# Performance work log

Measured on AMD Instinct MI355X. Metric: run time of the kernel, lower is better.

## Reference

```python
import jax, jax.numpy as jnp
import numpy as np

B, N, K, OUT = 8, 2048, 30, 13


def _knn_idx(x, k):
    # x: [B,N,F] -> indices of k nearest neighbors (squared L2, includes self)
    sq = jnp.sum(x * x, axis=-1)  # [B,N]
    d = sq[:, :, None] + sq[:, None, :] - 2.0 * jnp.einsum('bnf,bmf->bnm', x, x)
    _, idx = jax.lax.top_k(-d, k)  # [B,N,k]
    return idx


def _edge_conv(x, W1, b1, g, be, W2, b2, k):
    # DynamicEdgeConv: kNN on feature space, message = MLP([x_i, x_j - x_i]), max aggr
    idx = _knn_idx(x, k)                                  # [B,N,k] (non-differentiable)
    xj = jax.vmap(lambda xb, ib: xb[ib])(x, idx)          # gather neighbors [B,N,k,F]
    xi = x[:, :, None, :]
    e = jnp.concatenate([jnp.broadcast_to(xi, xj.shape), xj - xi], axis=-1)  # [B,N,k,2F]
    # PyG MLP([2F,64,64]): Linear + BN(eval: affine) + ReLU, then plain Linear
    h = jax.nn.relu((e @ W1 + b1) * g + be)
    h = h @ W2 + b2
    return jnp.max(h, axis=2)                             # max over k neighbors -> [B,N,64]


def setup_inputs():
    key = jax.random.key(0)
    ks = jax.random.split(key, 40)

    def lin(i, fin, fout):
        W = jax.random.normal(ks[i], (fin, fout), jnp.float32) / np.sqrt(fin)
        return W, jnp.zeros((fout,), jnp.float32)

    inp = {}
    inp['x'] = jax.random.normal(ks[0], (B, N, 3), jnp.float32)
    inp['pos'] = jax.random.normal(ks[1], (B, N, 3), jnp.float32)
    inp['batch'] = jnp.repeat(jnp.arange(B, dtype=jnp.int32), N)
    i = 2
    for name, fin in [('c1', 12), ('c2', 128), ('c3', 128)]:
        W1, b1 = lin(i, fin, 64); i += 1
        W2, b2 = lin(i, 64, 64); i += 1
        inp[name + '_W1'] = W1; inp[name + '_b1'] = b1
        inp[name + '_g'] = 1.0 + 0.1 * jax.random.normal(ks[i], (64,), jnp.float32); i += 1
        inp[name + '_be'] = 0.1 * jax.random.normal(ks[i], (64,), jnp.float32); i += 1
        inp[name + '_W2'] = W2; inp[name + '_b2'] = b2
    dims = [192, 1024, 256, 128, OUT]
    for j in range(4):
        W, b = lin(i, dims[j], dims[j + 1]); i += 1
        inp[f'm_W{j + 1}'] = W; inp[f'm_b{j + 1}'] = b
    return inp


def reference(x, pos, batch,
              c1_W1, c1_b1, c1_g, c1_be, c1_W2, c1_b2,
              c2_W1, c2_b1, c2_g, c2_be, c2_W2, c2_b2,
              c3_W1, c3_b1, c3_g, c3_be, c3_W2, c3_b2,
              m_W1, m_b1, m_W2, m_b2, m_W3, m_b3, m_W4, m_b4):
    x0 = jnp.concatenate([pos, x], axis=-1)               # [B,N,6]
    x1 = _edge_conv(x0, c1_W1, c1_b1, c1_g, c1_be, c1_W2, c1_b2, K)
    x2 = _edge_conv(x1, c2_W1, c2_b1, c2_g, c2_be, c2_W2, c2_b2, K)
    x3 = _edge_conv(x2, c3_W1, c3_b1, c3_g, c3_be, c3_W2, c3_b2, K)
    h = jnp.concatenate([x1, x2, x3], axis=-1)            # [B,N,192]
    # classifier MLP([192,1024,256,128,OUT], norm=None): Linear+ReLU(+dropout=eval id), plain last
    h = jax.nn.relu(h @ m_W1 + m_b1)
    h = jax.nn.relu(h @ m_W2 + m_b2)
    h = jax.nn.relu(h @ m_W3 + m_b3)
    out = h @ m_W4 + m_b4
    return jax.nn.log_softmax(out, axis=-1), x3
```

## Files before the change

kernel.cpp:

```cpp
#include <hip/hip_runtime.h>

using u16 = unsigned short;
using u32 = unsigned int;
typedef short s8v __attribute__((ext_vector_type(8)));
typedef short s4v __attribute__((ext_vector_type(4)));
typedef float f4v __attribute__((ext_vector_type(4)));

#define DEV static __device__ __forceinline__

DEV void cvt_split(float f, u16& h, u16& l) {
  u32 x = __builtin_bit_cast(u32, f);
  u32 rh = (x + 0x7FFFu + ((x >> 16) & 1u)) & 0xFFFF0000u;
  h = (u16)(rh >> 16);
  float fl = f - __builtin_bit_cast(float, rh);
  u32 y = __builtin_bit_cast(u32, fl);
  l = (u16)((y + 0x7FFFu + ((y >> 16) & 1u)) >> 16);
}

__global__ void k_misc0(const float* __restrict__ x, const float* __restrict__ pos,
                        float* __restrict__ x0,
                        const float* __restrict__ W2c3, u16* __restrict__ eW2h, u16* __restrict__ eW2l,
                        const float* __restrict__ W2c1, const float* __restrict__ W2c2,
                        float* __restrict__ W2T1, float* __restrict__ W2T2) {
  int b = blockIdx.x;
  if (b < 64) {
    int p = b * 256 + threadIdx.x;
    float* o = x0 + (size_t)p * 8;
    o[0] = pos[p*3+0]; o[1] = pos[p*3+1]; o[2] = pos[p*3+2];
    o[3] = x[p*3+0];   o[4] = x[p*3+1];   o[5] = x[p*3+2];
    o[6] = 0.f; o[7] = 0.f;
  } else if (b < 80) {
    int e = (b - 64) * 256 + threadIdx.x;
    int k = e >> 6, n = e & 63;
    u16 h, l;
    cvt_split(W2c3[e], h, l);
    eW2h[n*72 + k] = h;
    eW2l[n*72 + k] = l;
  } else {
    const float* src = (b == 80) ? W2c1 : W2c2;
    float* dst = (b == 80) ? W2T1 : W2T2;
    for (int e = threadIdx.x; e < 4096; e += 256) {
      int c = e >> 6, cp = e & 63;
      dst[cp*64 + c] = src[e];
    }
  }
}

__global__ void k_splitmlp(const float* __restrict__ W1, const float* __restrict__ W2,
                           const float* __restrict__ W3,
                           u16* __restrict__ m1h, u16* __restrict__ m1l,
                           u16* __restrict__ m2h, u16* __restrict__ m2l,
                           u16* __restrict__ m3h, u16* __restrict__ m3l) {
  int b = blockIdx.x;
  u16 h, l;
  if (b < 768) {
    int e = b * 256 + threadIdx.x;
    if (e < 192 * 1024) {
      int k = e >> 10, n = e & 1023;
      cvt_split(W1[e], h, l);
      m1h[(size_t)n*200 + k] = h; m1l[(size_t)n*200 + k] = l;
    }
  } else if (b < 1792) {
    int e = (b - 768) * 256 + threadIdx.x;
    int k = e >> 8, n = e & 255;
    cvt_split(W2[e], h, l);
    m2h[(size_t)n*1032 + k] = h; m2l[(size_t)n*1032 + k] = l;
  } else {
    int e = (b - 1792) * 256 + threadIdx.x;
    int k = e >> 7, n = e & 127;
    cvt_split(W3[e], h, l);
    m3h[(size_t)n*264 + k] = h; m3l[(size_t)n*264 + k] = l;
  }
}

__global__ void k_sqnorm(const float* __restrict__ x, int stride, int F,
                         float* __restrict__ sq) {
  int wid  = (blockIdx.x * 256 + threadIdx.x) >> 6;
  int lane = threadIdx.x & 63;
  float v = (lane < F) ? x[(size_t)wid * stride + lane] : 0.f;
  float s = v * v;
  #pragma unroll
  for (int m = 32; m; m >>= 1) s += __shfl_xor(s, m);
  if (lane == 0) sq[wid] = s;
}

template<int F>
__global__ __launch_bounds__(256) void k_dist(const float* __restrict__ x, int stride,
    const float* __restrict__ sq, int cbase, float* __restrict__ D) {
  constexpr int PAD = F + 4;
  __shared__ __align__(16) float Xi[128 * PAD];
  __shared__ __align__(16) float Xj[128 * PAD];
  __shared__ float SQI[128], SQJ[128];
  int b  = blockIdx.z;
  int i0 = cbase + blockIdx.y * 128;
  int j0 = blockIdx.x * 128;
  int tid = threadIdx.x;
  constexpr int NPASS = 128 * (F / 4) / 256;
  #pragma unroll
  for (int ps = 0; ps < NPASS; ++ps) {
    int e4 = ps * 256 + tid;
    int r = e4 / (F / 4), f4 = (e4 % (F / 4)) * 4;
    *(float4*)&Xi[r*PAD + f4] = *(const float4*)&x[(size_t)(b*2048 + i0 + r)*stride + f4];
    *(float4*)&Xj[r*PAD + f4] = *(const float4*)&x[(size_t)(b*2048 + j0 + r)*stride + f4];
  }
  if (tid < 128) {
    SQI[tid] = sq[b*2048 + i0 + tid];
    SQJ[tid] = sq[b*2048 + j0 + tid];
  }
  __syncthreads();
  int tx = tid & 15, ty = tid >> 4;
  float acc[8][8];
  #pragma unroll
  for (int i = 0; i < 8; ++i)
    #pragma unroll
    for (int j = 0; j < 8; ++j) acc[i][j] = 0.f;
  #pragma unroll 2
  for (int kf = 0; kf < F; kf += 4) {
    float4 av[8], wv[8];
    #pragma unroll
    for (int i = 0; i < 8; ++i) av[i] = *(const float4*)&Xi[(ty + 16*i)*PAD + kf];
    #pragma unroll
    for (int j = 0; j < 8; ++j) wv[j] = *(const float4*)&Xj[(tx + 16*j)*PAD + kf];
    #pragma unroll
    for (int i = 0; i < 8; ++i)
      #pragma unroll
      for (int j = 0; j < 8; ++j) {
        acc[i][j] += av[i].x * wv[j].x;
        acc[i][j] += av[i].y * wv[j].y;
        acc[i][j] += av[i].z * wv[j].z;
        acc[i][j] += av[i].w * wv[j].w;
      }
  }
  #pragma unroll
  for (int i = 0; i < 8; ++i) {
    int row = ty + 16*i;
    float si = SQI[row];
    #pragma unroll
    for (int j = 0; j < 8; ++j) {
      int col = tx + 16*j;
      D[(size_t)(b*512 + blockIdx.y*128 + row)*2048 + j0 + col] =
          si + SQJ[col] - 2.f * acc[i][j];
    }
  }
}

__global__ __launch_bounds__(256) void k_topk(const float* __restrict__ D, int cbase,
                                              int* __restrict__ knn) {
  int wid  = blockIdx.x * 4 + (threadIdx.x >> 6);
  int lane = threadIdx.x & 63;
  int b = wid >> 9, il = wid & 511;
  const float* row = D + (size_t)(b*512 + il) * 2048;
  float v[32];
  #pragma unroll
  for (int s = 0; s < 32; ++s) v[s] = row[lane + 64*s];
  const float INFV = __builtin_bit_cast(float, 0x7f800000u);
  int wj = 0;
  #pragma unroll 1
  for (int it = 0; it < 30; ++it) {
    float mv = v[0]; int ms = 0;
    #pragma unroll
    for (int s = 1; s < 32; ++s) {
      bool lt = v[s] < mv;
      mv = lt ? v[s] : mv;
      ms = lt ? s : ms;
    }
    int mj = lane + (ms << 6);
    #pragma unroll
    for (int m = 1; m < 64; m <<= 1) {
      float ov = __shfl_xor(mv, m);
      int   oj = __shfl_xor(mj, m);
      bool take = (ov < mv) || ((ov == mv) && (oj < mj));
      mv = take ? ov : mv;
      mj = take ? oj : mj;
    }
    int gj = __builtin_amdgcn_readfirstlane(mj);
    if (lane == it) wj = gj;
    int owner = gj & 63, slot = gj >> 6;
    #pragma unroll
    for (int s = 0; s < 32; ++s) {
      if (slot == s) {
        if (lane == owner) v[s] = INFV;
      }
    }
  }
  if (lane < 30) knn[(size_t)(b*2048 + cbase + il)*30 + lane] = b*2048 + wj;
}

__global__ __launch_bounds__(256) void k_prep(const float* __restrict__ x, int stride, int F,
    const float* __restrict__ W1, const float* __restrict__ b1,
    float* __restrict__ A0, float* __restrict__ V) {
  int p = blockIdx.x * 4 + (threadIdx.x >> 6);
  int lane = threadIdx.x & 63;
  float u = 0.f, v = 0.f;
  for (int f = 0; f < F; ++f) {
    float xv = x[(size_t)p*stride + f];
    float wa = W1[f*64 + lane];
    float wb = W1[(F + f)*64 + lane];
    u += xv * (wa - wb);
    v += xv * wb;
  }
  A0[p*64 + lane] = u + b1[lane];
  V[p*64 + lane]  = v;
}

__global__ __launch_bounds__(256) void k_edge_w(const float* __restrict__ A0,
    const float* __restrict__ V, const int* __restrict__ knn,
    const float* __restrict__ W2T, const float* __restrict__ b2,
    const float* __restrict__ g, const float* __restrict__ be,
    float* __restrict__ out, int ostride) {
  __shared__ float h2s[8][32][65];
  int wave = threadIdx.x >> 6, lane = threadIdx.x & 63;
  int half = lane >> 5, k = lane & 31;
  int kk = k < 30 ? k : 29;
  int pl = wave * 2 + half;
  int p  = blockIdx.x * 8 + pl;
  int j  = knn[(size_t)p * 30 + kk];

  float h1[64];
  const float* vr  = V  + (size_t)j * 64;
  const float* a0r = A0 + (size_t)p * 64;
  #pragma unroll
  for (int c = 0; c < 64; ++c) {
    float pre = (a0r[c] + vr[c]) * g[c] + be[c];
    h1[c] = pre > 0.f ? pre : 0.f;
  }
  #pragma unroll 1
  for (int cp = 0; cp < 64; ++cp) {
    const float* w = W2T + cp * 64;
    float s0 = 0.f, s1 = 0.f, s2 = 0.f, s3 = 0.f;
    #pragma unroll
    for (int c = 0; c < 64; c += 4) {
      s0 += h1[c+0] * w[c+0];
      s1 += h1[c+1] * w[c+1];
      s2 += h1[c+2] * w[c+2];
      s3 += h1[c+3] * w[c+3];
    }
    h2s[pl][k][cp] = (s0 + s1) + (s2 + s3);
  }
  __syncthreads();
  #pragma unroll
  for (int hh = 0; hh < 2; ++hh) {
    int pp = wave * 2 + hh;
    float m = h2s[pp][0][lane];
    #pragma unroll
    for (int t = 1; t < 30; ++t) m = fmaxf(m, h2s[pp][t][lane]);
    out[(size_t)(blockIdx.x * 8 + pp) * ostride + lane] = m + b2[lane];
  }
}

__global__ __launch_bounds__(256) void k_edge_m(const float* __restrict__ A0,
    const float* __restrict__ V, const int* __restrict__ knn,
    const u16* __restrict__ W2h, const u16* __restrict__ W2l,
    const float* __restrict__ b2,
    const float* __restrict__ g, const float* __restrict__ be,
    float* __restrict__ out, int ostride) {
  constexpr int PKW = 72;
  int p = blockIdx.x * 4 + (threadIdx.x >> 6);
  int lane = threadIdx.x & 63;
  int lr = lane & 15, kb = lane >> 4;

  const int* kr = knn + (size_t)p * 30;
  int j0 = kr[lr];
  int j1 = kr[lr + 16 < 30 ? lr + 16 : 29];

  s8v bh[4][2], bl[4][2];
  #pragma unroll
  for (int jf = 0; jf < 4; ++jf) {
    int n = jf*16 + lr;
    #pragma unroll
    for (int ks = 0; ks < 2; ++ks) {
      bh[jf][ks] = *(const s8v*)&W2h[n*PKW + ks*32 + kb*8];
      bl[jf][ks] = *(const s8v*)&W2l[n*PKW + ks*32 + kb*8];
    }
  }

  float base[2][8], gs[2][8];
  #pragma unroll
  for (int ks = 0; ks < 2; ++ks) {
    int cb = ks*32 + kb*8;
    float4 a0 = *(const float4*)&A0[(size_t)p*64 + cb];
    float4 a1 = *(const float4*)&A0[(size_t)p*64 + cb + 4];
    float4 g0 = *(const float4*)&g[cb];
    float4 g1 = *(const float4*)&g[cb + 4];
    float4 e0 = *(const float4*)&be[cb];
    float4 e1 = *(const float4*)&be[cb + 4];
    base[ks][0]=a0.x*g0.x+e0.x; base[ks][1]=a0.y*g0.y+e0.y;
    base[ks][2]=a0.z*g0.z+e0.z; base[ks][3]=a0.w*g0.w+e0.w;
    base[ks][4]=a1.x*g1.x+e1.x; base[ks][5]=a1.y*g1.y+e1.y;
    base[ks][6]=a1.z*g1.z+e1.z; base[ks][7]=a1.w*g1.w+e1.w;
    gs[ks][0]=g0.x; gs[ks][1]=g0.y; gs[ks][2]=g0.z; gs[ks][3]=g0.w;
    gs[ks][4]=g1.x; gs[ks][5]=g1.y; gs[ks][6]=g1.z; gs[ks][7]=g1.w;
  }

  s8v ah[2][2], al[2][2];
  #pragma unroll
  for (int mt = 0; mt < 2; ++mt) {
    const float* vr = V + (size_t)(mt ? j1 : j0) * 64;
    #pragma unroll
    for (int ks = 0; ks < 2; ++ks) {
      int cb = ks*32 + kb*8;
      float4 v0 = *(const float4*)&vr[cb];
      float4 v1 = *(const float4*)&vr[cb + 4];
      float hv[8];
      hv[0]=base[ks][0]+v0.x*gs[ks][0]; hv[1]=base[ks][1]+v0.y*gs[ks][1];
      hv[2]=base[ks][2]+v0.z*gs[ks][2]; hv[3]=base[ks][3]+v0.w*gs[ks][3];
      hv[4]=base[ks][4]+v1.x*gs[ks][4]; hv[5]=base[ks][5]+v1.y*gs[ks][5];
      hv[6]=base[ks][6]+v1.z*gs[ks][6]; hv[7]=base[ks][7]+v1.w*gs[ks][7];
      s8v hfrag, lfrag;
      #pragma unroll
      for (int e = 0; e < 8; ++e) {
        float h1 = hv[e] > 0.f ? hv[e] : 0.f;
        u16 hh, ll;
        cvt_split(h1, hh, ll);
        hfrag[e] = (short)hh; lfrag[e] = (short)ll;
      }
      ah[mt][ks] = hfrag; al[mt][ks] = lfrag;
    }
  }

  f4v acc[2][4];
  #pragma unroll
  for (int mt = 0; mt < 2; ++mt)
    #pragma unroll
    for (int jf = 0; jf < 4; ++jf) acc[mt][jf] = (f4v)(0.f);

  #pragma unroll
  for (int mt = 0; mt < 2; ++mt)
    #pragma unroll
    for (int jf = 0; jf < 4; ++jf)
      #pragma unroll
      for (int ks = 0; ks < 2; ++ks) {
        acc[mt][jf] = __builtin_amdgcn_mfma_f32_16x16x32_bf16(ah[mt][ks], bh[jf][ks], acc[mt][jf], 0, 0, 0);
        acc[mt][jf] = __builtin_amdgcn_mfma_f32_16x16x32_bf16(ah[mt][ks], bl[jf][ks], acc[mt][jf], 0, 0, 0);
        acc[mt][jf] = __builtin_amdgcn_mfma_f32_16x16x32_bf16(al[mt][ks], bh[jf][ks], acc[mt][jf], 0, 0, 0);
      }

  #pragma unroll
  for (int jf = 0; jf < 4; ++jf) {
    float m = fmaxf(fmaxf(acc[0][jf][0], acc[0][jf][1]), fmaxf(acc[0][jf][2], acc[0][jf][3]));
    float m1 = fmaxf(fmaxf(acc[1][jf][0], acc[1][jf][1]), fmaxf(acc[1][jf][2], acc[1][jf][3]));
    m = fmaxf(m, m1);
    m = fmaxf(m, __shfl_xor(m, 16));
    m = fmaxf(m, __shfl_xor(m, 32));
    if (kb == 0) out[(size_t)p*ostride + jf*16 + lr] = m + b2[jf*16 + lr];
  }
}

template<int NJF>
__global__ __launch_bounds__(256) void k_mlp(const float* __restrict__ Ag, int lda,
    const u16* __restrict__ Wth, const u16* __restrict__ Wtl, int PKW,
    const float* __restrict__ bg,
    float* __restrict__ Cg, int ldc, int N, int K, int dorelu) {
  constexpr int PK = 40;
  __shared__ __align__(16) u16 Ah[128*PK];
  __shared__ __align__(16) u16 Al[128*PK];
  int tid  = threadIdx.x;
  int wave = tid >> 6, lane = tid & 63;
  int wm = (wave >> 1) * 64, wn = (wave & 1) * (NJF*16);
  int lr = lane & 15, kb = lane >> 4;
  int m0 = blockIdx.y * 128, n0 = blockIdx.x * (2*NJF*16);

  f4v acc[4][NJF];
  #pragma unroll
  for (int i = 0; i < 4; ++i)
    #pragma unroll
    for (int j = 0; j < NJF; ++j) acc[i][j] = (f4v)(0.f);

  for (int k0 = 0; k0 < K; k0 += 32) {
    s8v bh[NJF], bl[NJF];
    #pragma unroll
    for (int jf = 0; jf < NJF; ++jf) {
      int n = n0 + wn + jf*16 + lr;
      bh[jf] = *(const s8v*)&Wth[(size_t)n*PKW + k0 + kb*8];
      bl[jf] = *(const s8v*)&Wtl[(size_t)n*PKW + k0 + kb*8];
    }
    #pragma unroll
    for (int ps = 0; ps < 4; ++ps) {
      int e4 = ps * 256 + tid;
      int r = e4 >> 3, c4 = (e4 & 7) << 2;
      float4 a = *(const float4*)&Ag[(size_t)(m0 + r)*lda + k0 + c4];
      u16 h0,h1,h2,h3,l0,l1,l2,l3;
      cvt_split(a.x, h0, l0); cvt_split(a.y, h1, l1);
      cvt_split(a.z, h2, l2); cvt_split(a.w, h3, l3);
      *(s4v*)&Ah[r*PK + c4] = s4v{(short)h0,(short)h1,(short)h2,(short)h3};
      *(s4v*)&Al[r*PK + c4] = s4v{(short)l0,(short)l1,(short)l2,(short)l3};
    }
    __syncthreads();
    #pragma unroll
    for (int mf = 0; mf < 4; ++mf) {
      int m = wm + mf*16 + lr;
      s8v ah = *(const s8v*)&Ah[m*PK + kb*8];
      s8v al = *(const s8v*)&Al[m*PK + kb*8];
      #pragma unroll
      for (int jf = 0; jf < NJF; ++jf) {
        acc[mf][jf] = __builtin_amdgcn_mfma_f32_16x16x32_bf16(ah, bh[jf], acc[mf][jf], 0, 0, 0);
        acc[mf][jf] = __builtin_amdgcn_mfma_f32_16x16x32_bf16(ah, bl[jf], acc[mf][jf], 0, 0, 0);
        acc[mf][jf] = __builtin_amdgcn_mfma_f32_16x16x32_bf16(al, bh[jf], acc[mf][jf], 0, 0, 0);
      }
    }
    __syncthreads();
  }

  #pragma unroll
  for (int jf = 0; jf < NJF; ++jf) {
    int n = n0 + wn + jf*16 + lr;
    float bb = bg[n];
    #pragma unroll
    for (int mf = 0; mf < 4; ++mf) {
      #pragma unroll
      for (int r = 0; r < 4; ++r) {
        int m = m0 + wm + mf*16 + kb*4 + r;
        float v = acc[mf][jf][r] + bb;
        if (dorelu) v = v > 0.f ? v : 0.f;
        Cg[(size_t)m*ldc + n] = v;
      }
    }
  }
}

__global__ __launch_bounds__(256) void k_head(const float* __restrict__ H3,
    const float* __restrict__ W4, const float* __restrict__ b4,
    float* __restrict__ out0, int pbase) {
  __shared__ float w4s[128 * 13];
  __shared__ float b4s[13];
  for (int e = threadIdx.x; e < 128*13; e += 256) w4s[e] = W4[e];
  if (threadIdx.x < 13) b4s[threadIdx.x] = b4[threadIdx.x];
  __syncthreads();
  int pl = blockIdx.x * 256 + threadIdx.x;
  float acc[13];
  #pragma unroll
  for (int c = 0; c < 13; ++c) acc[c] = b4s[c];
  const float* hr = H3 + (size_t)pl * 128;
  #pragma unroll 1
  for (int k = 0; k < 128; k += 4) {
    float4 h = *(const float4*)&hr[k];
    #pragma unroll
    for (int c = 0; c < 13; ++c) {
      acc[c] += h.x * w4s[(k+0)*13 + c];
      acc[c] += h.y * w4s[(k+1)*13 + c];
      acc[c] += h.z * w4s[(k+2)*13 + c];
      acc[c] += h.w * w4s[(k+3)*13 + c];
    }
  }
  float mx = acc[0];
  #pragma unroll
  for (int c = 1; c < 13; ++c) mx = fmaxf(mx, acc[c]);
  float s = 0.f;
  #pragma unroll
  for (int c = 0; c < 13; ++c) s += expf(acc[c] - mx);
  float lg = logf(s);
  size_t ob = (size_t)(pbase + pl) * 13;
  #pragma unroll
  for (int c = 0; c < 13; ++c) out0[ob + c] = acc[c] - mx - lg;
}

__global__ void k_out1(const float* __restrict__ hcat, float* __restrict__ out1) {
  int e = blockIdx.x * 256 + threadIdx.x;
  int p = e >> 6, c = e & 63;
  out1[e] = hcat[(size_t)p*192 + 128 + c];
}

extern "C" void kernel_launch(void* const* d_in, const int* in_sizes, int n_in,
                              void* d_out, int out_size, void* d_ws, size_t ws_size,
                              hipStream_t stream) {
  (void)in_sizes; (void)n_in; (void)out_size; (void)ws_size;
  const float* x   = (const float*)d_in[0];
  const float* pos = (const float*)d_in[1];
  const float* cw[3][6];
  for (int c = 0; c < 3; ++c)
    for (int t = 0; t < 6; ++t)
      cw[c][t] = (const float*)d_in[3 + c*6 + t];
  const float *mW[4], *mb[4];
  for (int j = 0; j < 4; ++j) {
    mW[j] = (const float*)d_in[21 + 2*j];
    mb[j] = (const float*)d_in[22 + 2*j];
  }

  float* ws   = (float*)d_ws;
  float* x0   = ws;
  float* sq   = x0 + 131072;
  int*   knn  = (int*)(sq + 16384);
  float* A0   = (float*)(knn + 491520);
  float* V    = A0 + 1048576;
  float* hcat = V + 1048576;
  float* U    = hcat + 3145728;
  float* H2c  = U + 8388608;
  float* H3c  = H2c + 2097152;
  float* W2T1 = H3c + 1048576;
  float* W2T2 = W2T1 + 4096;
  u16*   eW2  = (u16*)(W2T2 + 4096);
  u16* mwp = (u16*)A0;
  u16* m1h = mwp;            u16* m1l = m1h + 204800;
  u16* m2h = m1l + 204800;   u16* m2l = m2h + 264192;
  u16* m3h = m2l + 264192;   u16* m3l = m3h + 33792;

  float* out0 = (float*)d_out;
  float* out1 = out0 + 8*2048*13;

  k_misc0<<<82, 256, 0, stream>>>(x, pos, x0, cw[2][4], eW2, eW2 + 4608,
                                  cw[0][4], cw[1][4], W2T1, W2T2);

  for (int c = 0; c < 3; ++c) {
    const float* xin; int stride, F, Fsq;
    if (c == 0)      { xin = x0;        stride = 8;   F = 6;  Fsq = 8;  }
    else if (c == 1) { xin = hcat;      stride = 192; F = 64; Fsq = 64; }
    else             { xin = hcat + 64; stride = 192; F = 64; Fsq = 64; }
    k_sqnorm<<<4096, 256, 0, stream>>>(xin, stride, Fsq, sq);
    for (int ch = 0; ch < 4; ++ch) {
      if (c == 0) k_dist<8> <<<dim3(16,4,8), 256, 0, stream>>>(xin, stride, sq, ch*512, U);
      else        k_dist<64><<<dim3(16,4,8), 256, 0, stream>>>(xin, stride, sq, ch*512, U);
      k_topk<<<1024, 256, 0, stream>>>(U, ch*512, knn);
    }
    k_prep<<<4096, 256, 0, stream>>>(xin, stride, F, cw[c][0], cw[c][1], A0, V);
    if (c < 2)
      k_edge_w<<<2048, 256, 0, stream>>>(A0, V, knn, c == 0 ? W2T1 : W2T2,
                                         cw[c][5], cw[c][2], cw[c][3], hcat + 64*c, 192);
    else
      k_edge_m<<<4096, 256, 0, stream>>>(A0, V, knn, eW2, eW2 + 4608,
                                         cw[c][5], cw[c][2], cw[c][3], hcat + 64*c, 192);
  }

  k_splitmlp<<<1920, 256, 0, stream>>>(mW[0], mW[1], mW[2], m1h, m1l, m2h, m2l, m3h, m3l);

  for (int ch = 0; ch < 2; ++ch) {
    const float* Ain = hcat + (size_t)ch * 8192 * 192;
    k_mlp<4><<<dim3(8,64), 256, 0, stream>>>(Ain, 192,  m1h, m1l, 200,  mb[0], U,   1024, 1024, 192,  1);
    k_mlp<2><<<dim3(4,64), 256, 0, stream>>>(U,   1024, m2h, m2l, 1032, mb[1], H2c, 256,  256,  1024, 1);
    k_mlp<2><<<dim3(2,64), 256, 0, stream>>>(H2c, 256,  m3h, m3l, 264,  mb[2], H3c, 128,  128,  256,  1);
    k_head<<<32, 256, 0, stream>>>(H3c, mW[3], mb[3], out0, ch*8192);
  }
  k_out1<<<4096, 256, 0, stream>>>(hcat, out1);
}
```

Measured before the change: 1.411 ms.

## Pre-split MLP activations to bf16 hi/lo in epilogues and restructure edge conv

```diff
diff --git a/kernel.cpp b/kernel.cpp
--- a/kernel.cpp
+++ b/kernel.cpp
@@ -3,7 +3,6 @@
 using u16 = unsigned short;
 using u32 = unsigned int;
 typedef short s8v __attribute__((ext_vector_type(8)));
-typedef short s4v __attribute__((ext_vector_type(4)));
 typedef float f4v __attribute__((ext_vector_type(4)));
 
 #define DEV static __device__ __forceinline__
@@ -19,9 +18,7 @@
 
 __global__ void k_misc0(const float* __restrict__ x, const float* __restrict__ pos,
                         float* __restrict__ x0,
-                        const float* __restrict__ W2c3, u16* __restrict__ eW2h, u16* __restrict__ eW2l,
-                        const float* __restrict__ W2c1, const float* __restrict__ W2c2,
-                        float* __restrict__ W2T1, float* __restrict__ W2T2) {
+                        const float* __restrict__ W2c3, u16* __restrict__ eW2h, u16* __restrict__ eW2l) {
   int b = blockIdx.x;
   if (b < 64) {
     int p = b * 256 + threadIdx.x;
@@ -29,20 +26,13 @@
     o[0] = pos[p*3+0]; o[1] = pos[p*3+1]; o[2] = pos[p*3+2];
     o[3] = x[p*3+0];   o[4] = x[p*3+1];   o[5] = x[p*3+2];
     o[6] = 0.f; o[7] = 0.f;
-  } else if (b < 80) {
+  } else {
     int e = (b - 64) * 256 + threadIdx.x;
     int k = e >> 6, n = e & 63;
     u16 h, l;
     cvt_split(W2c3[e], h, l);
     eW2h[n*72 + k] = h;
     eW2l[n*72 + k] = l;
-  } else {
-    const float* src = (b == 80) ? W2c1 : W2c2;
-    float* dst = (b == 80) ? W2T1 : W2T2;
-    for (int e = threadIdx.x; e < 4096; e += 256) {
-      int c = e >> 6, cp = e & 63;
-      dst[cp*64 + c] = src[e];
-    }
   }
 }
 
@@ -73,6 +63,13 @@
   }
 }
 
+__global__ void k_splita(const float* __restrict__ A, u16* __restrict__ Ah, u16* __restrict__ Al) {
+  int e = blockIdx.x * 256 + threadIdx.x;
+  u16 h, l;
+  cvt_split(A[e], h, l);
+  Ah[e] = h; Al[e] = l;
+}
+
 __global__ void k_sqnorm(const float* __restrict__ x, int stride, int F,
                          float* __restrict__ sq) {
   int wid  = (blockIdx.x * 256 + threadIdx.x) >> 6;
@@ -203,49 +200,47 @@
   V[p*64 + lane]  = v;
 }
 
-__global__ __launch_bounds__(256) void k_edge_w(const float* __restrict__ A0,
+__global__ __launch_bounds__(256) void k_edge_b(const float* __restrict__ A0,
     const float* __restrict__ V, const int* __restrict__ knn,
-    const float* __restrict__ W2T, const float* __restrict__ b2,
+    const float* __restrict__ W2, const float* __restrict__ b2,
     const float* __restrict__ g, const float* __restrict__ be,
     float* __restrict__ out, int ostride) {
-  __shared__ float h2s[8][32][65];
+  __shared__ __align__(16) float h1s[4][30][68];
   int wave = threadIdx.x >> 6, lane = threadIdx.x & 63;
-  int half = lane >> 5, k = lane & 31;
-  int kk = k < 30 ? k : 29;
-  int pl = wave * 2 + half;
-  int p  = blockIdx.x * 8 + pl;
-  int j  = knn[(size_t)p * 30 + kk];
-
-  float h1[64];
-  const float* vr  = V  + (size_t)j * 64;
-  const float* a0r = A0 + (size_t)p * 64;
-  #pragma unroll
-  for (int c = 0; c < 64; ++c) {
-    float pre = (a0r[c] + vr[c]) * g[c] + be[c];
-    h1[c] = pre > 0.f ? pre : 0.f;
-  }
+  int p = blockIdx.x * 4 + wave;
+
+  float w2c[64];
+  #pragma unroll
+  for (int c = 0; c < 64; ++c) w2c[c] = W2[c*64 + lane];
+
+  float a0 = A0[(size_t)p*64 + lane];
+  float gg = g[lane], bbe = be[lane];
+  const int* kr = knn + (size_t)p*30;
+
+  #pragma unroll 2
+  for (int k = 0; k < 30; ++k) {
+    int j = kr[k];
+    float v = V[(size_t)j*64 + lane];
+    float pre = (a0 + v) * gg + bbe;
+    h1s[wave][k][lane] = pre > 0.f ? pre : 0.f;
+  }
+
+  float m = -3.0e38f;
   #pragma unroll 1
-  for (int cp = 0; cp < 64; ++cp) {
-    const float* w = W2T + cp * 64;
+  for (int k = 0; k < 30; ++k) {
     float s0 = 0.f, s1 = 0.f, s2 = 0.f, s3 = 0.f;
     #pragma unroll
     for (int c = 0; c < 64; c += 4) {
-      s0 += h1[c+0] * w[c+0];
-      s1 += h1[c+1] * w[c+1];
-      s2 += h1[c+2] * w[c+2];
-      s3 += h1[c+3] * w[c+3];
-    }
-    h2s[pl][k][cp] = (s0 + s1) + (s2 + s3);
-  }
-  __syncthreads();
-  #pragma unroll
-  for (int hh = 0; hh < 2; ++hh) {
-    int pp = wave * 2 + hh;
-    float m = h2s[pp][0][lane];
-    #pragma unroll
-    for (int t = 1; t < 30; ++t) m = fmaxf(m, h2s[pp][t][lane]);
-    out[(size_t)(blockIdx.x * 8 + pp) * ostride + lane] = m + b2[lane];
-  }
+      float4 hv = *(const float4*)&h1s[wave][k][c];
+      s0 += hv.x * w2c[c+0];
+      s1 += hv.y * w2c[c+1];
+      s2 += hv.z * w2c[c+2];
+      s3 += hv.w * w2c[c+3];
+    }
+    float h2 = (s0 + s1) + (s2 + s3);
+    m = m > h2 ? m : h2;
+  }
+  out[(size_t)p*ostride + lane] = m + b2[lane];
 }
 
 __global__ __launch_bounds__(256) void k_edge_m(const float* __restrict__ A0,
@@ -346,14 +341,13 @@
   }
 }
 
-template<int NJF>
-__global__ __launch_bounds__(256) void k_mlp(const float* __restrict__ Ag, int lda,
+template<int NJF, int SPLIT>
+__global__ __launch_bounds__(256) void k_mlp(
+    const u16* __restrict__ Ahg, const u16* __restrict__ Alg, int lka,
     const u16* __restrict__ Wth, const u16* __restrict__ Wtl, int PKW,
     const float* __restrict__ bg,
-    float* __restrict__ Cg, int ldc, int N, int K, int dorelu) {
-  constexpr int PK = 40;
-  __shared__ __align__(16) u16 Ah[128*PK];
-  __shared__ __align__(16) u16 Al[128*PK];
+    float* __restrict__ Cf, u16* __restrict__ Ch, u16* __restrict__ Cl,
+    int ldc, int K) {
   int tid  = threadIdx.x;
   int wave = tid >> 6, lane = tid & 63;
   int wm = (wave >> 1) * 64, wn = (wave & 1) * (NJF*16);
@@ -367,7 +361,7 @@
     for (int j = 0; j < NJF; ++j) acc[i][j] = (f4v)(0.f);
 
   for (int k0 = 0; k0 < K; k0 += 32) {
-    s8v bh[NJF], bl[NJF];
+    s8v bh[NJF], bl[NJF], ah[4], al[4];
     #pragma unroll
     for (int jf = 0; jf < NJF; ++jf) {
       int n = n0 + wn + jf*16 + lr;
@@ -375,30 +369,19 @@
       bl[jf] = *(const s8v*)&Wtl[(size_t)n*PKW + k0 + kb*8];
     }
     #pragma unroll
-    for (int ps = 0; ps < 4; ++ps) {
-      int e4 = ps * 256 + tid;
-      int r = e4 >> 3, c4 = (e4 & 7) << 2;
-      float4 a = *(const float4*)&Ag[(size_t)(m0 + r)*lda + k0 + c4];
-      u16 h0,h1,h2,h3,l0,l1,l2,l3;
-      cvt_split(a.x, h0, l0); cvt_split(a.y, h1, l1);
-      cvt_split(a.z, h2, l2); cvt_split(a.w, h3, l3);
-      *(s4v*)&Ah[r*PK + c4] = s4v{(short)h0,(short)h1,(short)h2,(short)h3};
-      *(s4v*)&Al[r*PK + c4] = s4v{(short)l0,(short)l1,(short)l2,(short)l3};
-    }
-    __syncthreads();
-    #pragma unroll
     for (int mf = 0; mf < 4; ++mf) {
-      int m = wm + mf*16 + lr;
-      s8v ah = *(const s8v*)&Ah[m*PK + kb*8];
-      s8v al = *(const s8v*)&Al[m*PK + kb*8];
+      size_t a = (size_t)(m0 + wm + mf*16 + lr)*lka + k0 + kb*8;
+      ah[mf] = *(const s8v*)&Ahg[a];
+      al[mf] = *(const s8v*)&Alg[a];
+    }
+    #pragma unroll
+    for (int mf = 0; mf < 4; ++mf)
       #pragma unroll
       for (int jf = 0; jf < NJF; ++jf) {
-        acc[mf][jf] = __builtin_amdgcn_mfma_f32_16x16x32_bf16(ah, bh[jf], acc[mf][jf], 0, 0, 0);
-        acc[mf][jf] = __builtin_amdgcn_mfma_f32_16x16x32_bf16(ah, bl[jf], acc[mf][jf], 0, 0, 0);
-        acc[mf][jf] = __builtin_amdgcn_mfma_f32_16x16x32_bf16(al, bh[jf], acc[mf][jf], 0, 0, 0);
+        acc[mf][jf] = __builtin_amdgcn_mfma_f32_16x16x32_bf16(ah[mf], bh[jf], acc[mf][jf], 0, 0, 0);
+        acc[mf][jf] = __builtin_amdgcn_mfma_f32_16x16x32_bf16(ah[mf], bl[jf], acc[mf][jf], 0, 0, 0);
+        acc[mf][jf] = __builtin_amdgcn_mfma_f32_16x16x32_bf16(al[mf], bh[jf], acc[mf][jf], 0, 0, 0);
       }
-    }
-    __syncthreads();
   }
 
   #pragma unroll
@@ -411,8 +394,15 @@
       for (int r = 0; r < 4; ++r) {
         int m = m0 + wm + mf*16 + kb*4 + r;
         float v = acc[mf][jf][r] + bb;
-        if (dorelu) v = v > 0.f ? v : 0.f;
-        Cg[(size_t)m*ldc + n] = v;
+        v = v > 0.f ? v : 0.f;
+        if (SPLIT) {
+          u16 h, l;
+          cvt_split(v, h, l);
+          Ch[(size_t)m*ldc + n] = h;
+          Cl[(size_t)m*ldc + n] = l;
+        } else {
+          Cf[(size_t)m*ldc + n] = v;
+        }
       }
     }
   }
@@ -486,19 +476,21 @@
   float* U    = hcat + 3145728;
   float* H2c  = U + 8388608;
   float* H3c  = H2c + 2097152;
-  float* W2T1 = H3c + 1048576;
-  float* W2T2 = W2T1 + 4096;
-  u16*   eW2  = (u16*)(W2T2 + 4096);
-  u16* mwp = (u16*)A0;
+  u16*   eW2  = (u16*)(H3c + 1048576);
+
+  u16* mwp = (u16*)(V + 524288);
   u16* m1h = mwp;            u16* m1l = m1h + 204800;
   u16* m2h = m1l + 204800;   u16* m2l = m2h + 264192;
   u16* m3h = m2l + 264192;   u16* m3l = m3h + 33792;
+  u16* Aih = (u16*)A0;
+  u16* Ail = Aih + 1572864;
+  u16* H1h = (u16*)U;        u16* H1l = H1h + 8388608;
+  u16* H2h = (u16*)H2c;      u16* H2l = H2h + 2097152;
 
   float* out0 = (float*)d_out;
   float* out1 = out0 + 8*2048*13;
 
-  k_misc0<<<82, 256, 0, stream>>>(x, pos, x0, cw[2][4], eW2, eW2 + 4608,
-                                  cw[0][4], cw[1][4], W2T1, W2T2);
+  k_misc0<<<80, 256, 0, stream>>>(x, pos, x0, cw[2][4], eW2, eW2 + 4608);
 
   for (int c = 0; c < 3; ++c) {
     const float* xin; int stride, F, Fsq;
@@ -513,8 +505,8 @@
     }
     k_prep<<<4096, 256, 0, stream>>>(xin, stride, F, cw[c][0], cw[c][1], A0, V);
     if (c < 2)
-      k_edge_w<<<2048, 256, 0, stream>>>(A0, V, knn, c == 0 ? W2T1 : W2T2,
-                                         cw[c][5], cw[c][2], cw[c][3], hcat + 64*c, 192);
+      k_edge_b<<<4096, 256, 0, stream>>>(A0, V, knn, cw[c][4], cw[c][5],
+                                         cw[c][2], cw[c][3], hcat + 64*c, 192);
     else
       k_edge_m<<<4096, 256, 0, stream>>>(A0, V, knn, eW2, eW2 + 4608,
                                          cw[c][5], cw[c][2], cw[c][3], hcat + 64*c, 192);
@@ -523,10 +515,13 @@
   k_splitmlp<<<1920, 256, 0, stream>>>(mW[0], mW[1], mW[2], m1h, m1l, m2h, m2l, m3h, m3l);
 
   for (int ch = 0; ch < 2; ++ch) {
-    const float* Ain = hcat + (size_t)ch * 8192 * 192;
-    k_mlp<4><<<dim3(8,64), 256, 0, stream>>>(Ain, 192,  m1h, m1l, 200,  mb[0], U,   1024, 1024, 192,  1);
-    k_mlp<2><<<dim3(4,64), 256, 0, stream>>>(U,   1024, m2h, m2l, 1032, mb[1], H2c, 256,  256,  1024, 1);
-    k_mlp<2><<<dim3(2,64), 256, 0, stream>>>(H2c, 256,  m3h, m3l, 264,  mb[2], H3c, 128,  128,  256,  1);
+    k_splita<<<6144, 256, 0, stream>>>(hcat + (size_t)ch * 8192 * 192, Aih, Ail);
+    k_mlp<4,1><<<dim3(8,64), 256, 0, stream>>>(Aih, Ail, 192,  m1h, m1l, 200,  mb[0],
+                                               nullptr, H1h, H1l, 1024, 192);
+    k_mlp<2,1><<<dim3(4,64), 256, 0, stream>>>(H1h, H1l, 1024, m2h, m2l, 1032, mb[1],
+                                               nullptr, H2h, H2l, 256, 1024);
+    k_mlp<2,0><<<dim3(2,64), 256, 0, stream>>>(H2h, H2l, 256,  m3h, m3l, 264,  mb[2],
+                                               H3c, nullptr, nullptr, 128, 256);
     k_head<<<32, 256, 0, stream>>>(H3c, mW[3], mb[3], out0, ch*8192);
   }
   k_out1<<<4096, 256, 0, stream>>>(hcat, out1);
```

Measured after the change: 1.375 ms. 1.03x faster.
